# Kernel tuning notes

Measured on AMD Instinct MI355X. Metric: run time of the kernel, lower is better.

Reference implementation:

```python
import jax, jax.numpy as jnp
import numpy as np

BATCH = 16384
N = 4096


def setup_inputs() -> dict:
    key = jax.random.key(0)
    kx, kw = jax.random.split(key)
    x = jax.random.normal(kx, (BATCH, N), dtype=jnp.float32)
    first_row = jax.random.normal(kw, (N,), dtype=jnp.float32) * 0.1
    return {"x": x, "first_row": first_row}


def reference(x, first_row):
    # Circulant matmul via FFT: y = ifft(fft(x) * fft(w)).real
    # fft_weights broadcast over batch dim. Inputs are real, so the
    # complex FFTs are Hermitian-symmetric and the ifft is real up to
    # rounding; original module takes .real, matched here.
    fft_w = jnp.fft.fft(first_row)          # (N,) complex64
    fft_x = jnp.fft.fft(x)                  # (BATCH, N) complex64
    out = jnp.fft.ifft(fft_x * fft_w).real  # (BATCH, N) float32
    return out
```

## Files before the change

kernel.cpp:

```cpp
#include <hip/hip_runtime.h>

#define FFT_N 4096
#define NT 256
#define NPAD(i) ((i) + ((i) >> 4))
#define LDS_SZ (FFT_N + (FFT_N >> 4))

struct cf { float x, y; };

__device__ __forceinline__ cf cadd(cf a, cf b) { return cf{a.x + b.x, a.y + b.y}; }
__device__ __forceinline__ cf csub(cf a, cf b) { return cf{a.x - b.x, a.y - b.y}; }
__device__ __forceinline__ cf cmul(cf a, cf b) {
    return cf{a.x * b.x - a.y * b.y, a.x * b.y + a.y * b.x};
}
template <int DIR> __device__ __forceinline__ cf muli(cf a) {
    if constexpr (DIR < 0) return cf{a.y, -a.x};
    else                   return cf{-a.y, a.x};
}

template <int DIR> __device__ __forceinline__ void dft16(cf v[16]) {
#pragma unroll
    for (int s = 0; s < 4; ++s) {
        cf t0 = cadd(v[s], v[s + 8]);
        cf t1 = csub(v[s], v[s + 8]);
        cf t2 = cadd(v[s + 4], v[s + 12]);
        cf t3 = csub(v[s + 4], v[s + 12]);
        cf m3 = muli<DIR>(t3);
        v[s]      = cadd(t0, t2);
        v[s + 8]  = csub(t0, t2);
        v[s + 4]  = cadd(t1, m3);
        v[s + 12] = csub(t1, m3);
    }
    constexpr float C1 = 0.9238795325112867f;
    constexpr float S1 = 0.3826834323650898f;
    constexpr float R2 = 0.7071067811865476f;
    constexpr float sg = (DIR < 0) ? -1.0f : 1.0f;
    const cf w1 = cf{C1, sg * S1};
    const cf w2 = cf{R2, sg * R2};
    const cf w3 = cf{S1, sg * C1};
    const cf w6 = cf{-R2, sg * R2};
    const cf w9 = cf{-C1, -sg * S1};
    v[5]  = cmul(v[5], w1);
    v[9]  = cmul(v[9], w2);
    v[13] = cmul(v[13], w3);
    v[6]  = cmul(v[6], w2);
    v[10] = muli<DIR>(v[10]);
    v[14] = cmul(v[14], w6);
    v[7]  = cmul(v[7], w3);
    v[11] = cmul(v[11], w6);
    v[15] = cmul(v[15], w9);
    cf o[16];
#pragma unroll
    for (int p = 0; p < 4; ++p) {
        cf t0 = cadd(v[4 * p + 0], v[4 * p + 2]);
        cf t1 = csub(v[4 * p + 0], v[4 * p + 2]);
        cf t2 = cadd(v[4 * p + 1], v[4 * p + 3]);
        cf t3 = csub(v[4 * p + 1], v[4 * p + 3]);
        cf m3 = muli<DIR>(t3);
        o[p]      = cadd(t0, t2);
        o[8 + p]  = csub(t0, t2);
        o[4 + p]  = cadd(t1, m3);
        o[12 + p] = csub(t1, m3);
    }
#pragma unroll
    for (int k = 0; k < 16; ++k) v[k] = o[k];
}

template <int DIR>
__device__ __forceinline__ void fft4096(cf v[16], float* __restrict__ lre,
                                        float* __restrict__ lim, int j) {
    dft16<DIR>(v);
    __syncthreads();
#pragma unroll
    for (int r = 0; r < 16; ++r) {
        int a = NPAD(j * 16 + r);
        lre[a] = v[r].x;
        lim[a] = v[r].y;
    }
    __syncthreads();
#pragma unroll
    for (int r = 0; r < 16; ++r) {
        int a = NPAD(j + 256 * r);
        v[r].x = lre[a];
        v[r].y = lim[a];
    }
    {
        float th = (float)DIR * 6.283185307179586f * (float)(j & 15) * (1.0f / 256.0f);
        float sn, cs;
        __sincosf(th, &sn, &cs);
        cf wb = cf{cs, sn};
        cf wr = wb;
#pragma unroll
        for (int r = 1; r < 16; ++r) {
            v[r] = cmul(v[r], wr);
            wr = cmul(wr, wb);
        }
    }
    dft16<DIR>(v);
    __syncthreads();
#pragma unroll
    for (int r = 0; r < 16; ++r) {
        int a = NPAD((j >> 4) * 256 + (j & 15) + 16 * r);
        lre[a] = v[r].x;
        lim[a] = v[r].y;
    }
    __syncthreads();
#pragma unroll
    for (int r = 0; r < 16; ++r) {
        int a = NPAD(j + 256 * r);
        v[r].x = lre[a];
        v[r].y = lim[a];
    }
    {
        float th = (float)DIR * 6.283185307179586f * (float)j * (1.0f / 4096.0f);
        float sn, cs;
        __sincosf(th, &sn, &cs);
        cf wb = cf{cs, sn};
        cf wr = wb;
#pragma unroll
        for (int r = 1; r < 16; ++r) {
            v[r] = cmul(v[r], wr);
            wr = cmul(wr, wb);
        }
    }
    dft16<DIR>(v);
}

__global__ void __launch_bounds__(NT) fftw_kernel(const float* __restrict__ w,
                                                  float2* __restrict__ W) {
    __shared__ float lre[LDS_SZ];
    __shared__ float lim[LDS_SZ];
    int j = threadIdx.x;
    cf v[16];
#pragma unroll
    for (int r = 0; r < 16; ++r) {
        v[r].x = w[j + 256 * r];
        v[r].y = 0.0f;
    }
    fft4096<-1>(v, lre, lim, j);
    const float inv = 1.0f / (float)FFT_N;
#pragma unroll
    for (int r = 0; r < 16; ++r) {
        W[j + 256 * r] = make_float2(v[r].x * inv, v[r].y * inv);
    }
}

__global__ void __launch_bounds__(NT) circulant_main(const float* __restrict__ x,
                                                     const float2* __restrict__ W,
                                                     float* __restrict__ y) {
    __shared__ float lre[LDS_SZ];
    __shared__ float lim[LDS_SZ];
    int j = threadIdx.x;
    long long base = (long long)blockIdx.x * 2LL * FFT_N;
    const float* x0 = x + base;
    const float* x1 = x0 + FFT_N;
    cf v[16];
#pragma unroll
    for (int r = 0; r < 16; ++r) {
        v[r].x = x0[j + 256 * r];
        v[r].y = x1[j + 256 * r];
    }
    fft4096<-1>(v, lre, lim, j);
#pragma unroll
    for (int r = 0; r < 16; ++r) {
        float2 wv = W[j + 256 * r];
        v[r] = cmul(v[r], cf{wv.x, wv.y});
    }
    fft4096<1>(v, lre, lim, j);
    float* y0 = y + base;
    float* y1 = y0 + FFT_N;
#pragma unroll
    for (int r = 0; r < 16; ++r) {
        y0[j + 256 * r] = v[r].x;
        y1[j + 256 * r] = v[r].y;
    }
}

extern "C" void kernel_launch(void* const* d_in, const int* in_sizes, int n_in,
                              void* d_out, int out_size, void* d_ws, size_t ws_size,
                              hipStream_t stream) {
    const float* x = (const float*)d_in[0];
    const float* first_row = (const float*)d_in[1];
    float* y = (float*)d_out;
    float2* W = (float2*)d_ws;

    hipLaunchKernelGGL(fftw_kernel, dim3(1), dim3(NT), 0, stream, first_row, W);
    hipLaunchKernelGGL(circulant_main, dim3(16384 / 2), dim3(NT), 0, stream, x, W, y);
}
```

Measured before the change: 448.5 us.

## Interleave complex LDS storage with new padding and tree-based twiddle generation

Replaces the split real/imaginary shared-memory arrays with one interleaved float2 array using a different padding scheme. This allows 128-bit vector stores in the first transpose and 64-bit accesses elsewhere, which cuts the number of LDS instructions. Twiddle powers are now built with a squaring tree instead of a serial chain, giving a shorter dependency chain and possibly better accuracy. LDS footprint grows from about 34KB to 40KB per block, which may reduce occupancy, and the new padding may change bank-conflict behaviour.

```diff
diff --git a/kernel.cpp b/kernel.cpp
--- a/kernel.cpp
+++ b/kernel.cpp
@@ -2,8 +2,8 @@
 
 #define FFT_N 4096
 #define NT 256
-#define NPAD(i) ((i) + ((i) >> 4))
-#define LDS_SZ (FFT_N + (FFT_N >> 4))
+#define PADC(s) ((s) + 2 * ((s) >> 3))
+#define LDS_CF 5120
 
 struct cf { float x, y; };
 
@@ -65,70 +65,70 @@
     for (int k = 0; k < 16; ++k) v[k] = o[k];
 }
 
+__device__ __forceinline__ void twiddle16(cf v[16], float th) {
+    float sn, cs;
+    __sincosf(th, &sn, &cs);
+    cf w[16];
+    w[1] = cf{cs, sn};
+    w[2] = cmul(w[1], w[1]);
+    w[3] = cmul(w[2], w[1]);
+#pragma unroll
+    for (int k = 2; k < 8; ++k) {
+        w[2 * k]     = cmul(w[k], w[k]);
+        w[2 * k + 1] = cmul(w[k], w[k + 1]);
+    }
+#pragma unroll
+    for (int r = 1; r < 16; ++r) v[r] = cmul(v[r], w[r]);
+}
+
 template <int DIR>
-__device__ __forceinline__ void fft4096(cf v[16], float* __restrict__ lre,
-                                        float* __restrict__ lim, int j) {
+__device__ __forceinline__ void fft4096(cf v[16], float2* __restrict__ lds2, int j) {
+    constexpr float TPI = 6.283185307179586f;
     dft16<DIR>(v);
     __syncthreads();
+    {
+        int b = 20 * j;
 #pragma unroll
-    for (int r = 0; r < 16; ++r) {
-        int a = NPAD(j * 16 + r);
-        lre[a] = v[r].x;
-        lim[a] = v[r].y;
+        for (int r = 0; r < 16; r += 2) {
+            int a = b + r + 2 * (r >> 3);
+            float4 pk = make_float4(v[r].x, v[r].y, v[r + 1].x, v[r + 1].y);
+            *reinterpret_cast<float4*>(&lds2[a]) = pk;
+        }
     }
     __syncthreads();
+    {
+        int b = j + 2 * (j >> 3);
 #pragma unroll
-    for (int r = 0; r < 16; ++r) {
-        int a = NPAD(j + 256 * r);
-        v[r].x = lre[a];
-        v[r].y = lim[a];
-    }
-    {
-        float th = (float)DIR * 6.283185307179586f * (float)(j & 15) * (1.0f / 256.0f);
-        float sn, cs;
-        __sincosf(th, &sn, &cs);
-        cf wb = cf{cs, sn};
-        cf wr = wb;
-#pragma unroll
-        for (int r = 1; r < 16; ++r) {
-            v[r] = cmul(v[r], wr);
-            wr = cmul(wr, wb);
+        for (int r = 0; r < 16; ++r) {
+            float2 t = lds2[b + 320 * r];
+            v[r] = cf{t.x, t.y};
         }
     }
+    twiddle16(v, (float)DIR * TPI * (float)(j & 15) * (1.0f / 256.0f));
     dft16<DIR>(v);
     __syncthreads();
+    {
+        int b = 320 * (j >> 4) + (j & 15) + 2 * ((j & 15) >> 3);
 #pragma unroll
-    for (int r = 0; r < 16; ++r) {
-        int a = NPAD((j >> 4) * 256 + (j & 15) + 16 * r);
-        lre[a] = v[r].x;
-        lim[a] = v[r].y;
+        for (int r = 0; r < 16; ++r)
+            lds2[b + 20 * r] = make_float2(v[r].x, v[r].y);
     }
     __syncthreads();
+    {
+        int b = j + 2 * (j >> 3);
 #pragma unroll
-    for (int r = 0; r < 16; ++r) {
-        int a = NPAD(j + 256 * r);
-        v[r].x = lre[a];
-        v[r].y = lim[a];
-    }
-    {
-        float th = (float)DIR * 6.283185307179586f * (float)j * (1.0f / 4096.0f);
-        float sn, cs;
-        __sincosf(th, &sn, &cs);
-        cf wb = cf{cs, sn};
-        cf wr = wb;
-#pragma unroll
-        for (int r = 1; r < 16; ++r) {
-            v[r] = cmul(v[r], wr);
-            wr = cmul(wr, wb);
+        for (int r = 0; r < 16; ++r) {
+            float2 t = lds2[b + 320 * r];
+            v[r] = cf{t.x, t.y};
         }
     }
+    twiddle16(v, (float)DIR * TPI * (float)j * (1.0f / 4096.0f));
     dft16<DIR>(v);
 }
 
 __global__ void __launch_bounds__(NT) fftw_kernel(const float* __restrict__ w,
                                                   float2* __restrict__ W) {
-    __shared__ float lre[LDS_SZ];
-    __shared__ float lim[LDS_SZ];
+    __shared__ __align__(16) float2 lds2[LDS_CF];
     int j = threadIdx.x;
     cf v[16];
 #pragma unroll
@@ -136,7 +136,7 @@
         v[r].x = w[j + 256 * r];
         v[r].y = 0.0f;
     }
-    fft4096<-1>(v, lre, lim, j);
+    fft4096<-1>(v, lds2, j);
     const float inv = 1.0f / (float)FFT_N;
 #pragma unroll
     for (int r = 0; r < 16; ++r) {
@@ -147,8 +147,7 @@
 __global__ void __launch_bounds__(NT) circulant_main(const float* __restrict__ x,
                                                      const float2* __restrict__ W,
                                                      float* __restrict__ y) {
-    __shared__ float lre[LDS_SZ];
-    __shared__ float lim[LDS_SZ];
+    __shared__ __align__(16) float2 lds2[LDS_CF];
     int j = threadIdx.x;
     long long base = (long long)blockIdx.x * 2LL * FFT_N;
     const float* x0 = x + base;
@@ -159,13 +158,13 @@
         v[r].x = x0[j + 256 * r];
         v[r].y = x1[j + 256 * r];
     }
-    fft4096<-1>(v, lre, lim, j);
+    fft4096<-1>(v, lds2, j);
 #pragma unroll
     for (int r = 0; r < 16; ++r) {
         float2 wv = W[j + 256 * r];
         v[r] = cmul(v[r], cf{wv.x, wv.y});
     }
-    fft4096<1>(v, lre, lim, j);
+    fft4096<1>(v, lds2, j);
     float* y0 = y + base;
     float* y1 = y0 + FFT_N;
 #pragma unroll
```

Measured after the change: 444.1 us. No clear change (-1.0%).
